# Optimization experiments

Hardware: AMD Instinct MI355X
Metric: run time of the kernel (lower is better)

Reference implementation:

```python
import jax, jax.numpy as jnp
import numpy as np

N, P, VEC, M = 100000, 96, 4, 70000
GROUPS = [27, 8, 8]
K = sum(GROUPS)  # 43
# Replicates the original's use of the LOCAL per-group offset index i_k when
# selecting attention weights in the output accumulation loop.
ATTN_IDX = np.concatenate([np.arange(g) for g in GROUPS]).astype(np.int32)


def setup_inputs() -> dict:
    key = jax.random.key(0)
    ks = jax.random.split(key, 12)
    rng = np.random.default_rng(0)
    # Kernel maps: per offset, M (in_idx, out_idx) pairs; out indices unique per
    # offset (each output point has at most one neighbor at a given offset).
    kmaps = np.stack([
        np.stack([rng.integers(0, N, M), rng.permutation(N)[:M]], axis=1)
        for _ in range(K)
    ]).astype(np.int32)  # [K, M, 2]
    w = lambda k, shape: jax.random.normal(k, shape, jnp.float32) * 0.05
    return dict(
        x=w(ks[0], (N, P)),
        coords=jax.random.uniform(ks[1], (N, 3), jnp.float32, 0.0, 100.0),
        Wq1=w(ks[2], (27, P, P)), gq1=jnp.ones(P), bq1=jnp.zeros(P),
        Wq2=w(ks[3], (27, P, VEC)), gq2=jnp.ones(VEC), bq2=jnp.zeros(VEC),
        Wv=w(ks[4], (27, P, P)), gv=jnp.ones(P), bv=jnp.zeros(P),
        Wp1=w(ks[5], (3, P)), gp1=jnp.ones(P), bp1=jnp.zeros(P),
        Wp2=w(ks[6], (P, VEC)), gp2=jnp.ones(VEC), bp2=jnp.zeros(VEC),
        W1=w(ks[7], (VEC, P)), b1=jnp.zeros(P),
        W2=w(ks[8], (P, VEC)), b2=jnp.zeros(VEC),
        g_out=jnp.ones(P), b_out=jnp.zeros(P),
        kmaps=jnp.asarray(kmaps),
    )


def _bn(x, g, b, eps=1e-5):
    m = x.mean(0)
    v = x.var(0)
    return g * (x - m) * jax.lax.rsqrt(v + eps) + b


def _sparse_conv3(x, W, km27, n):
    # Minkowski kernel-size-3 sparse conv: out[dst] += x[src] @ W[k] per offset.
    def step(acc, kw):
        km, Wk = kw
        return acc.at[km[:, 1]].add(x[km[:, 0]] @ Wk), None
    out, _ = jax.lax.scan(step, jnp.zeros((n, W.shape[-1]), x.dtype), (km27, W))
    return out


def _cbr(x, W, g, b, km27, n):
    return jax.nn.relu(_bn(_sparse_conv3(x, W, km27, n), g, b))


def _forward(x, coords, Wq1, gq1, bq1, Wq2, gq2, bq2, Wv, gv, bv,
             Wp1, gp1, bp1, Wp2, gp2, bp2, W1, b1, W2, b2, g_out, b_out, kmaps):
    n, p = x.shape
    rep = p // VEC  # expand_vec_dim factor
    km27 = kmaps[:27]
    # q branch: two conv3-BN-ReLU stages -> [N, VEC]
    qf = _cbr(_cbr(x, Wq1, gq1, bq1, km27, n), Wq2, gq2, bq2, km27, n)
    # v branch: conv3-BN-ReLU -> [N, P]
    vf = _cbr(x, Wv, gv, bv, km27, n)
    # positional encoding: two 1x1 conv-BN-ReLU on coords -> [N, VEC] -> [N, P]
    pe = jax.nn.relu(_bn(jax.nn.relu(_bn(coords @ Wp1, gp1, bp1)) @ Wp2, gp2, bp2))
    v_f = vf + jnp.repeat(pe, rep, axis=1)

    def attn_step(carry, km):
        src, dst = km[:, 0], km[:, 1]
        # presence mask of offset-k neighbors (scatter of x features, zero elsewhere)
        sm = jnp.zeros((n, p), x.dtype).at[dst].set(x[src])
        mask = jax.lax.stop_gradient((jnp.abs(sm).sum(-1) > 0).astype(x.dtype))  # [N]
        gq = jnp.zeros((n, VEC), x.dtype).at[dst].set(qf[src])
        d = gq - qf * mask[:, None]
        logits = (jax.nn.relu(d @ W1 + b1) @ W2 + b2) * mask[:, None]
        return carry, (logits, mask)

    _, (logits, masks) = jax.lax.scan(attn_step, None, kmaps)  # [K,N,VEC], [K,N]
    attn = jax.nn.softmax(logits, axis=0)  # softmax across the K stacked offsets
    attn_sel = attn[jnp.asarray(ATTN_IDX)]  # replicate local-index selection bug

    def out_step(acc, inp):
        km, mask, a = inp
        nv = jnp.zeros((n, p), x.dtype).at[km[:, 1]].set(v_f[km[:, 0]]) * mask[:, None]
        return acc + nv * jnp.repeat(a, rep, axis=1), None

    out, _ = jax.lax.scan(out_step, jnp.zeros((n, p), x.dtype),
                          (kmaps, masks, attn_sel))
    # out BN + ReLU, residual (inplanes == planes so res = x)
    return jax.nn.relu(_bn(out, g_out, b_out)) + x


def reference(x, coords, Wq1, gq1, bq1, Wq2, gq2, bq2, Wv, gv, bv,
              Wp1, gp1, bp1, Wp2, gp2, bp2, W1, b1, W2, b2, g_out, b_out, kmaps):
    return _forward(x, coords, Wq1, gq1, bq1, Wq2, gq2, bq2, Wv, gv, bv,
                    Wp1, gp1, bp1, Wp2, gp2, bp2, W1, b1, W2, b2,
                    g_out, b_out, kmaps)
```

## Files before the change

kernel.cpp:

```cpp
#include <hip/hip_runtime.h>
#include <math.h>

#define N_  100000
#define P_  96
#define V_  4
#define M_  70000
#define K_  43
#define KC_ 27

typedef unsigned short u16;
typedef __attribute__((ext_vector_type(8))) short bf16x8;
typedef __attribute__((ext_vector_type(4))) float f32x4;
typedef __attribute__((ext_vector_type(16))) float f32x16;

__device__ __forceinline__ u16 f2bf(float f) {
    unsigned int u = __float_as_uint(f);
    u += 0x7fffu + ((u >> 16) & 1u);
    return (u16)(u >> 16);
}
__device__ __forceinline__ float bf2f(u16 h) {
    return __uint_as_float(((unsigned int)h) << 16);
}

__device__ __forceinline__ void gl_lds16(const u16* g, u16* l) {
    __builtin_amdgcn_global_load_lds(
        (const __attribute__((address_space(1))) void*)g,
        (__attribute__((address_space(3))) void*)l, 16, 0, 0);
}

__global__ __launch_bounds__(256) void k_build_srcof(const int* __restrict__ km,
                                                     int* __restrict__ srcOf) {
    int idx = blockIdx.x * 256 + threadIdx.x;
    if (idx >= K_ * M_) return;
    int k = idx / M_;
    int e = idx - k * M_;
    const int* p = km + (size_t)(k * M_ + e) * 2;
    srcOf[(size_t)k * N_ + p[1]] = p[0];
}

__global__ __launch_bounds__(256) void k_rowabs_cvt(const float* __restrict__ x,
                                                    float* __restrict__ rowAbs,
                                                    u16* __restrict__ xb) {
    int row = blockIdx.x * 4 + (threadIdx.x >> 6);
    int lane = threadIdx.x & 63;
    if (row >= N_) return;
    const float* xr = x + (size_t)row * 96;
    float s = 0.f;
    for (int j = lane; j < 96; j += 64) {
        float v = xr[j];
        s += fabsf(v);
        xb[(size_t)row * 96 + j] = f2bf(v);
    }
#pragma unroll
    for (int o = 32; o > 0; o >>= 1) s += __shfl_down(s, o, 64);
    if (lane == 0) rowAbs[row] = s;
}

__global__ __launch_bounds__(256) void k_wt96p(const float* __restrict__ W,
                                               u16* __restrict__ Wp) {
    int idx = blockIdx.x * 256 + threadIdx.x;
    if (idx >= KC_ * 96 * 96) return;
    int k = idx / 9216, rem = idx - k * 9216, n = rem / 96, j = rem - n * 96;
    Wp[(size_t)k * 10240 + n * 104 + j] = f2bf(W[(size_t)k * 9216 + j * 96 + n]);
}

__global__ __launch_bounds__(256) void k_wtB(const float* __restrict__ W,
                                             u16* __restrict__ Bimg) {
    int idx = blockIdx.x * 256 + threadIdx.x;
    if (idx >= 128 * 104) return;
    int n = idx / 104, j = idx - n * 104;
    u16 v = 0;
    if (j < 96 && n < 108) {
        int ks = n >> 2, c = n & 3;
        v = f2bf(W[(size_t)ks * 384 + j * 4 + c]);
    }
    Bimg[idx] = v;
}

__global__ __launch_bounds__(256) void k_w12b(const float* __restrict__ W1,
                                              const float* __restrict__ W2,
                                              u16* __restrict__ w1b,
                                              u16* __restrict__ w2b) {
    int t = blockIdx.x * 256 + threadIdx.x;
    if (t < 96 * 32) {
        int j = t >> 5, c = t & 31;
        w1b[t] = (c < 4) ? f2bf(W1[c * 96 + j]) : (u16)0;
    }
    if (t < 16 * 96) {
        int n = t / 96, j = t - n * 96;
        w2b[t] = (n < 4) ? f2bf(W2[j * 4 + n]) : (u16)0;
    }
}

__global__ __launch_bounds__(384, 3) void k_conv96_dual(
    const u16* __restrict__ xb, const u16* __restrict__ Wqp,
    const u16* __restrict__ Wvp, const int* __restrict__ srcOf,
    u16* __restrict__ yQ, u16* __restrict__ yV,
    float* __restrict__ statsQ, float* __restrict__ statsV) {
    __shared__ u16 sA[192 * 104];
    __shared__ u16 sBq[10240];
    __shared__ u16 sBv[10240];
    const int r0 = blockIdx.x * 192;
    const int t = threadIdx.x;
    const int wv = t / 64, lane = t & 63;
    const int n32 = lane & 31, half = lane >> 5;
    const int ea = t >> 1, jca = (t & 1) * 6;
    f32x16 accq[3], accv[3];
#pragma unroll
    for (int i = 0; i < 3; i++) {
#pragma unroll
        for (int j = 0; j < 16; j++) { accq[i][j] = 0.f; accv[i][j] = 0.f; }
    }

    for (int k = 0; k < KC_; k++) {
        __syncthreads();
        {
            const u16* gq = Wqp + (size_t)k * 10240;
            const u16* gv = Wvp + (size_t)k * 10240;
            for (int i = wv; i < 40; i += 6) {
                int mv = (i >= 20);
                int off = (mv ? i - 20 : i) * 512 + lane * 8;
                gl_lds16((mv ? gv : gq) + off, (mv ? (u16*)sBv : (u16*)sBq) + off);
            }
        }
        {
            int r = r0 + ea;
            int src = (r < N_) ? srcOf[(size_t)k * N_ + r] : -1;
            if (src >= 0) {
                const uint4* sp = (const uint4*)(xb + (size_t)src * 96);
#pragma unroll
                for (int i = 0; i < 6; i++)
                    *(uint4*)(sA + ea * 104 + (jca + i) * 8) = sp[jca + i];
            } else {
                uint4 z = make_uint4(0, 0, 0, 0);
#pragma unroll
                for (int i = 0; i < 6; i++)
                    *(uint4*)(sA + ea * 104 + (jca + i) * 8) = z;
            }
        }
        __syncthreads();
#pragma unroll
        for (int ks = 0; ks < 6; ks++) {
            bf16x8 af = *(const bf16x8*)(sA + (wv * 32 + n32) * 104 + ks * 16 + half * 8);
#pragma unroll
            for (int nt = 0; nt < 3; nt++) {
                bf16x8 bq = *(const bf16x8*)(sBq + (nt * 32 + n32) * 104 + ks * 16 + half * 8);
                accq[nt] = __builtin_amdgcn_mfma_f32_32x32x16_bf16(af, bq, accq[nt], 0, 0, 0);
                bf16x8 bv = *(const bf16x8*)(sBv + (nt * 32 + n32) * 104 + ks * 16 + half * 8);
                accv[nt] = __builtin_amdgcn_mfma_f32_32x32x16_bf16(af, bv, accv[nt], 0, 0, 0);
            }
        }
    }
#pragma unroll
    for (int nt = 0; nt < 3; nt++) {
#pragma unroll
        for (int reg = 0; reg < 16; reg++) {
            int row = (reg & 3) + 8 * (reg >> 2) + 4 * half;
            int r = r0 + wv * 32 + row;
            if (r < N_) {
                yQ[(size_t)r * 96 + nt * 32 + n32] = f2bf(accq[nt][reg]);
                yV[(size_t)r * 96 + nt * 32 + n32] = f2bf(accv[nt][reg]);
            }
        }
    }
    __syncthreads();
    float* sred = (float*)sA;
    for (int pass = 0; pass < 2; pass++) {
        f32x16* acc = pass ? accv : accq;
        float* st = pass ? statsV : statsQ;
#pragma unroll
        for (int nt = 0; nt < 3; nt++) {
            float sv = 0.f, qv = 0.f;
#pragma unroll
            for (int reg = 0; reg < 16; reg++) {
                float a = acc[nt][reg];
                sv += a; qv += a * a;
            }
            sv += __shfl_xor(sv, 32, 64);
            qv += __shfl_xor(qv, 32, 64);
            if (half == 0) {
                sred[wv * 192 + nt * 32 + n32] = sv;
                sred[wv * 192 + 96 + nt * 32 + n32] = qv;
            }
        }
        __syncthreads();
        if (t < 192) {
            float tot = 0.f;
#pragma unroll
            for (int w = 0; w < 6; w++) tot += sred[w * 192 + t];
            atomicAdd(&st[t], tot);
        }
        __syncthreads();
    }
}

__global__ __launch_bounds__(256) void k_proj(
    const u16* __restrict__ xq, const float* __restrict__ stats,
    const float* __restrict__ gg, const float* __restrict__ bb,
    const u16* __restrict__ Bimg, u16* __restrict__ gout) {
    __shared__ u16 sA[128 * 104];
    __shared__ u16 sB[128 * 104];
    __shared__ float sSc[96], sSh[96];
    const int r0 = blockIdx.x * 128;
    const int t = threadIdx.x;
    const int wv = t >> 6, lane = t & 63;
    const int n32 = lane & 31, half = lane >> 5;
    if (t < 96) {
        float mean = stats[t] * (1.f / N_);
        float var = stats[96 + t] * (1.f / N_) - mean * mean;
        float sc = gg[t] * rsqrtf(fmaxf(var, 0.f) + 1e-5f);
        sSc[t] = sc; sSh[t] = bb[t] - mean * sc;
    }
    for (int i = t; i < 1664; i += 256)
        ((uint4*)sB)[i] = ((const uint4*)Bimg)[i];
    __syncthreads();
    {
        int ea = t >> 1, jca = (t & 1) * 6;
        int r = r0 + ea;
        bool ok = (r < N_);
        const u16* xr = xq + (size_t)(ok ? r : 0) * 96;
#pragma unroll
        for (int i = 0; i < 6; i++) {
            int cb = (jca + i) * 8;
            uint4 v = ok ? *(const uint4*)(xr + cb) : make_uint4(0, 0, 0, 0);
            const u16* pv = (const u16*)&v;
            u16 o[8];
#pragma unroll
            for (int e = 0; e < 8; e++) {
                float h = bf2f(pv[e]);
                h = fmaxf(h * sSc[cb + e] + sSh[cb + e], 0.f);
                o[e] = f2bf(h);
            }
            *(uint4*)(sA + ea * 104 + cb) = *(uint4*)o;
        }
    }
    __syncthreads();
    f32x16 acc[4];
#pragma unroll
    for (int i = 0; i < 4; i++)
#pragma unroll
        for (int j = 0; j < 16; j++) acc[i][j] = 0.f;
#pragma unroll
    for (int ks = 0; ks < 6; ks++) {
        bf16x8 af = *(const bf16x8*)(sA + (wv * 32 + n32) * 104 + ks * 16 + half * 8);
#pragma unroll
        for (int nt = 0; nt < 4; nt++) {
            bf16x8 bf = *(const bf16x8*)(sB + (nt * 32 + n32) * 104 + ks * 16 + half * 8);
            acc[nt] = __builtin_amdgcn_mfma_f32_32x32x16_bf16(af, bf, acc[nt], 0, 0, 0);
        }
    }
#pragma unroll
    for (int nt = 0; nt < 4; nt++) {
        int col = nt * 32 + n32;
        if (col < 108) {
#pragma unroll
            for (int reg = 0; reg < 16; reg++) {
                int row = (reg & 3) + 8 * (reg >> 2) + 4 * half;
                int r = r0 + wv * 32 + row;
                if (r < N_) gout[(size_t)r * 108 + col] = f2bf(acc[nt][reg]);
            }
        }
    }
}

__global__ __launch_bounds__(256) void k_gather4(
    const u16* __restrict__ g, const int* __restrict__ srcOf,
    float* __restrict__ qf) {
    int idx = blockIdx.x * 256 + threadIdx.x;
    if (idx >= N_ * 4) return;
    int r = idx >> 2, c = idx & 3;
    float a = 0.f;
    int sv[9]; u16 gv[9];
#pragma unroll 1
    for (int kb = 0; kb < 27; kb += 9) {
#pragma unroll
        for (int j = 0; j < 9; j++)
            sv[j] = srcOf[(size_t)(kb + j) * N_ + r];
#pragma unroll
        for (int j = 0; j < 9; j++) {
            int sc = (sv[j] >= 0) ? sv[j] : 0;
            gv[j] = g[(size_t)sc * 108 + (kb + j) * 4 + c];
        }
#pragma unroll
        for (int j = 0; j < 9; j++)
            if (sv[j] >= 0) a += bf2f(gv[j]);
    }
    qf[idx] = a;
}

__global__ __launch_bounds__(192) void k_bnstats96(const float* __restrict__ xin,
                                                   float* __restrict__ stats) {
    __shared__ float sS[192], sQ[192];
    int t = threadIdx.x;
    int ch = t % 96, half = t / 96;
    float s = 0.f, q = 0.f;
    for (int r = blockIdx.x * 2 + half; r < N_; r += gridDim.x * 2) {
        float v = xin[(size_t)r * 96 + ch];
        s += v; q += v * v;
    }
    sS[t] = s; sQ[t] = q;
    __syncthreads();
    if (t < 96) {
        atomicAdd(&stats[ch], sS[t] + sS[t + 96]);
        atomicAdd(&stats[96 + ch], sQ[t] + sQ[t + 96]);
    }
}

__global__ __launch_bounds__(256) void k_bnstats4(const float* __restrict__ xin,
                                                  float* __restrict__ stats) {
    __shared__ float sS[256], sQ[256];
    int t = threadIdx.x;
    int c = t & 3, sub = t >> 2;
    float s = 0.f, q = 0.f;
    for (int r = blockIdx.x * 64 + sub; r < N_; r += gridDim.x * 64) {
        float v = xin[(size_t)r * 4 + c];
        s += v; q += v * v;
    }
    sS[t] = s; sQ[t] = q;
    __syncthreads();
    for (int off = 128; off >= 4; off >>= 1) {
        if (t < off) { sS[t] += sS[t + off]; sQ[t] += sQ[t + off]; }
        __syncthreads();
    }
    if (t < 4) {
        atomicAdd(&stats[t], sS[t]);
        atomicAdd(&stats[96 + t], sQ[t]);
    }
}

template <int C, int MODE>
__global__ __launch_bounds__(256) void k_bnapply(float* __restrict__ y,
                                                 const float* __restrict__ stats,
                                                 const float* __restrict__ g,
                                                 const float* __restrict__ b,
                                                 const float* __restrict__ aux) {
    int idx = blockIdx.x * 256 + threadIdx.x;
    if (idx >= N_ * C) return;
    int ch = idx % C;
    float mean = stats[ch] * (1.f / N_);
    float var = stats[96 + ch] * (1.f / N_) - mean * mean;
    float scale = g[ch] * rsqrtf(fmaxf(var, 0.f) + 1e-5f);
    float v = (y[idx] - mean) * scale + b[ch];
    v = fmaxf(v, 0.f);
    if (MODE == 2) v += aux[idx];
    y[idx] = v;
}

__global__ __launch_bounds__(256) void k_bnapply96_pe(
    const u16* __restrict__ yin, const float* __restrict__ stats,
    const float* __restrict__ g, const float* __restrict__ b,
    const float* __restrict__ aux, u16* __restrict__ yout) {
    int idx = blockIdx.x * 256 + threadIdx.x;
    if (idx >= N_ * 96) return;
    int ch = idx % 96;
    float mean = stats[ch] * (1.f / N_);
    float var = stats[96 + ch] * (1.f / N_) - mean * mean;
    float scale = g[ch] * rsqrtf(fmaxf(var, 0.f) + 1e-5f);
    float v = (bf2f(yin[idx]) - mean) * scale + b[ch];
    v = fmaxf(v, 0.f);
    int r = idx / 96;
    v += aux[(size_t)r * 4 + (ch / 24)];
    yout[idx] = f2bf(v);
}

__global__ __launch_bounds__(192) void k_pe1s(const float* __restrict__ coords,
                                              const float* __restrict__ Wp1,
                                              u16* __restrict__ out,
                                              float* __restrict__ stats) {
    __shared__ float sS[192], sQ[192];
    int t = threadIdx.x;
    int ch = t % 96, half = t / 96;
    float w0 = Wp1[ch], w1 = Wp1[96 + ch], w2 = Wp1[192 + ch];
    float s = 0.f, q = 0.f;
    for (int r = blockIdx.x * 2 + half; r < N_; r += gridDim.x * 2) {
        float c0 = coords[r * 3], c1 = coords[r * 3 + 1], c2 = coords[r * 3 + 2];
        float v = c0 * w0 + c1 * w1 + c2 * w2;
        out[(size_t)r * 96 + ch] = f2bf(v);
        s += v; q += v * v;
    }
    sS[t] = s; sQ[t] = q;
    __syncthreads();
    if (t < 96) {
        atomicAdd(&stats[ch], sS[t] + sS[t + 96]);
        atomicAdd(&stats[96 + ch], sQ[t] + sQ[t + 96]);
    }
}

__global__ __launch_bounds__(256) void k_pe2b(const u16* __restrict__ hin,
                                              const float* __restrict__ stats,
                                              const float* __restrict__ gp,
                                              const float* __restrict__ bp,
                                              const float* __restrict__ Wp2,
                                              float* __restrict__ out) {
    __shared__ float sSc[96], sSh[96], sW[384];
    int t = threadIdx.x;
    if (t < 96) {
        float mean = stats[t] * (1.f / N_);
        float var = stats[96 + t] * (1.f / N_) - mean * mean;
        float sc = gp[t] * rsqrtf(fmaxf(var, 0.f) + 1e-5f);
        sSc[t] = sc; sSh[t] = bp[t] - mean * sc;
    }
    for (int i = t; i < 384; i += 256) sW[i] = Wp2[i];
    __syncthreads();
    int idx = blockIdx.x * 256 + t;
    if (idx >= N_ * 4) return;
    int r = idx >> 2, c = idx & 3;
    const u16* hr = hin + (size_t)r * 96;
    float acc = 0.f;
#pragma unroll 4
    for (int j = 0; j < 96; j++) {
        float h = fmaxf(bf2f(hr[j]) * sSc[j] + sSh[j], 0.f);
        acc += h * sW[j * 4 + c];
    }
    out[idx] = acc;
}

__global__ __launch_bounds__(256) void k_attn_logits_mfma(
    const float* __restrict__ qf, const int* __restrict__ srcOf,
    const float* __restrict__ rowAbs,
    const u16* __restrict__ w1b, const float* __restrict__ b1,
    const u16* __restrict__ w2b, const float* __restrict__ b2,
    u16* __restrict__ wb) {
    __shared__ u16 hbuf[4][16 * 104];
    __shared__ u16 slogb[32][176];
    __shared__ u16 smk16[32][44];
    const int t = threadIdx.x;
    const int wv = t >> 6, lane = t & 63;
    const int col = lane & 15, quad = lane >> 4;
    const int r0 = blockIdx.x * 32;

    bf16x8 w1f[6];
    float b1v[6];
#pragma unroll
    for (int nt = 0; nt < 6; nt++) {
        w1f[nt] = *(const bf16x8*)(w1b + (nt * 16 + col) * 32 + quad * 8);
        b1v[nt] = b1[nt * 16 + col];
    }
    bf16x8 w2f[3];
#pragma unroll
    for (int kk = 0; kk < 3; kk++)
        w2f[kk] = *(const bf16x8*)(w2b + col * 96 + kk * 32 + quad * 8);
    float b2v = b2[col & 3];

    u16* hb = hbuf[wv];
    for (int tt = 0; tt < 22; tt++) {
        int tileBase = (wv * 22 + tt) * 16;
        bf16x8 af = (bf16x8){0, 0, 0, 0, 0, 0, 0, 0};
        if (quad == 0) {
            int P = tileBase + col;
            int rL = P / 44, k = P - rL * 44;
            int kc = (k < 43) ? k : 42;
            int r = r0 + rL;
            int s = srcOf[(size_t)kc * N_ + r];
            if (k == 43) s = -1;
            int sc = (s >= 0) ? s : 0;
            float mk = (s >= 0 && rowAbs[sc] > 0.f) ? 1.f : 0.f;
            float4 qs = *(const float4*)(qf + (size_t)sc * 4);
            float4 qr = *(const float4*)(qf + (size_t)r * 4);
            af[0] = (short)f2bf((qs.x - qr.x) * mk);
            af[1] = (short)f2bf((qs.y - qr.y) * mk);
            af[2] = (short)f2bf((qs.z - qr.z) * mk);
            af[3] = (short)f2bf((qs.w - qr.w) * mk);
            if (k < 43) smk16[rL][k] = (u16)(mk > 0.f ? 1 : 0);
        }
        f32x4 c1[6];
#pragma unroll
        for (int nt = 0; nt < 6; nt++) {
            c1[nt] = (f32x4){0.f, 0.f, 0.f, 0.f};
            c1[nt] = __builtin_amdgcn_mfma_f32_16x16x32_bf16(af, w1f[nt], c1[nt], 0, 0, 0);
        }
#pragma unroll
        for (int nt = 0; nt < 6; nt++) {
#pragma unroll
            for (int rg = 0; rg < 4; rg++) {
                float h = fmaxf(c1[nt][rg] + b1v[nt], 0.f);
                hb[(quad * 4 + rg) * 104 + nt * 16 + col] = f2bf(h);
            }
        }
        f32x4 acc2 = (f32x4){0.f, 0.f, 0.f, 0.f};
#pragma unroll
        for (int kk = 0; kk < 3; kk++) {
            bf16x8 a2 = *(const bf16x8*)(hb + col * 104 + kk * 32 + quad * 8);
            acc2 = __builtin_amdgcn_mfma_f32_16x16x32_bf16(a2, w2f[kk], acc2, 0, 0, 0);
        }
        if (col < 4) {
#pragma unroll
            for (int rg = 0; rg < 4; rg++) {
                int P = tileBase + quad * 4 + rg;
                int rL = P / 44, k = P - rL * 44;
                if (k < 43) {
                    float mval = (float)smk16[rL][k];
                    slogb[rL][k * 4 + col] = f2bf((acc2[rg] + b2v) * mval);
                }
            }
        }
    }
    __syncthreads();

    if (t < 128) {
        int rL = t >> 2, c = t & 3;
        float mx = 0.f;
        for (int k = 0; k < K_; k++) mx = fmaxf(mx, bf2f(slogb[rL][k * 4 + c]));
        float den = 0.f;
        for (int k = 0; k < K_; k++) den += __expf(bf2f(slogb[rL][k * 4 + c]) - mx);
        float inv = 1.f / den;
        for (int k = 0; k < K_; k++)
            slogb[rL][k * 4 + c] = f2bf(__expf(bf2f(slogb[rL][k * 4 + c]) - mx) * inv);
    }
    __syncthreads();

    for (int p = t; p < 32 * 43; p += 256) {
        int rL = p / 43, k = p - rL * 43;
        int idxk = (k < 27) ? k : ((k < 35) ? (k - 27) : (k - 35));
        u16 mk = smk16[rL][k];
        ushort4 wout = make_ushort4(0, 0, 0, 0);
        if (mk) {
            wout.x = slogb[rL][idxk * 4 + 0];
            wout.y = slogb[rL][idxk * 4 + 1];
            wout.z = slogb[rL][idxk * 4 + 2];
            wout.w = slogb[rL][idxk * 4 + 3];
        }
        *(ushort4*)(wb + ((size_t)(r0 + rL) * 44 + k) * 4) = wout;
    }
}

__global__ __launch_bounds__(256) void k_attn_gather(
    const u16* __restrict__ vfb, const u16* __restrict__ wb,
    const int* __restrict__ srcOf, float* __restrict__ out) {
    int idx = blockIdx.x * 256 + threadIdx.x;
    int r = idx / 24, c4 = idx - r * 24;
    if (r >= N_) return;
    int cg = c4 / 6;
    const u16* wrow = wb + (size_t)r * 176 + cg;
    float a0 = 0.f, a1 = 0.f, a2 = 0.f, a3 = 0.f;
    int sv[8]; float wv[8]; ushort4 vv[8];
#pragma unroll 1
    for (int kb = 0; kb < 40; kb += 8) {
#pragma unroll
        for (int j = 0; j < 8; j++)
            sv[j] = srcOf[(size_t)(kb + j) * N_ + r];
#pragma unroll
        for (int j = 0; j < 8; j++)
            wv[j] = bf2f(wrow[(size_t)(kb + j) * 4]);
#pragma unroll
        for (int j = 0; j < 8; j++) {
            int sc = (sv[j] >= 0) ? sv[j] : 0;
            vv[j] = *(const ushort4*)(vfb + (size_t)sc * 96 + c4 * 4);
        }
#pragma unroll
        for (int j = 0; j < 8; j++) {
            float w = (sv[j] >= 0) ? wv[j] : 0.f;
            a0 += w * bf2f(vv[j].x);
            a1 += w * bf2f(vv[j].y);
            a2 += w * bf2f(vv[j].z);
            a3 += w * bf2f(vv[j].w);
        }
    }
#pragma unroll
    for (int j = 0; j < 3; j++)
        sv[j] = srcOf[(size_t)(40 + j) * N_ + r];
#pragma unroll
    for (int j = 0; j < 3; j++)
        wv[j] = bf2f(wrow[(size_t)(40 + j) * 4]);
#pragma unroll
    for (int j = 0; j < 3; j++) {
        int sc = (sv[j] >= 0) ? sv[j] : 0;
        vv[j] = *(const ushort4*)(vfb + (size_t)sc * 96 + c4 * 4);
    }
#pragma unroll
    for (int j = 0; j < 3; j++) {
        float w = (sv[j] >= 0) ? wv[j] : 0.f;
        a0 += w * bf2f(vv[j].x);
        a1 += w * bf2f(vv[j].y);
        a2 += w * bf2f(vv[j].z);
        a3 += w * bf2f(vv[j].w);
    }
    *(float4*)(out + (size_t)r * 96 + c4 * 4) = make_float4(a0, a1, a2, a3);
}

extern "C" void kernel_launch(void* const* d_in, const int* in_sizes, int n_in,
                              void* d_out, int out_size, void* d_ws, size_t ws_size,
                              hipStream_t stream) {
    const float* x      = (const float*)d_in[0];
    const float* coords = (const float*)d_in[1];
    const float* Wq1 = (const float*)d_in[2];
    const float* gq1 = (const float*)d_in[3];
    const float* bq1 = (const float*)d_in[4];
    const float* Wq2 = (const float*)d_in[5];
    const float* gq2 = (const float*)d_in[6];
    const float* bq2 = (const float*)d_in[7];
    const float* Wv  = (const float*)d_in[8];
    const float* gv  = (const float*)d_in[9];
    const float* bv  = (const float*)d_in[10];
    const float* Wp1 = (const float*)d_in[11];
    const float* gp1 = (const float*)d_in[12];
    const float* bp1 = (const float*)d_in[13];
    const float* Wp2 = (const float*)d_in[14];
    const float* gp2 = (const float*)d_in[15];
    const float* bp2 = (const float*)d_in[16];
    const float* W1  = (const float*)d_in[17];
    const float* b1  = (const float*)d_in[18];
    const float* W2  = (const float*)d_in[19];
    const float* b2  = (const float*)d_in[20];
    const float* g_out = (const float*)d_in[21];
    const float* b_out = (const float*)d_in[22];
    const int* kmaps = (const int*)d_in[23];
    float* out = (float*)d_out;

    char* ws = (char*)d_ws;
    int*   srcOf  = (int*)ws;
    float* rowAbs = (float*)(ws + 17200000);
    u16*   xb     = (u16*)(ws + 17600000);
    u16*   pescr  = (u16*)(ws + 17600000);
    u16*   wbuf   = (u16*)(ws + 17600000);
    u16*   bufQb  = (u16*)(ws + 36800000);
    float* peb    = (float*)(ws + 36800000);
    u16*   Wq1p   = (u16*)(ws + 56000000);
    u16*   Wvp    = (u16*)(ws + 56552960);
    u16*   gbuf   = (u16*)(ws + 56000000);
    u16*   vfb    = (u16*)(ws + 56000000);
    u16*   bufVb  = (u16*)(ws + 77600000);
    u16*   Bimg   = (u16*)(ws + 96800000);
    float* qf     = (float*)(ws + 96800000);
    u16*   w1b    = (u16*)(ws + 98400000);
    u16*   w2b    = (u16*)(ws + 98406144);
    float* stats  = (float*)(ws + 98409216);

    hipMemsetAsync(srcOf, 0xFF, (size_t)K_ * N_ * 4, stream);
    hipMemsetAsync(stats, 0, 6 * 192 * 4, stream);

    k_build_srcof<<<(K_ * M_ + 255) / 256, 256, 0, stream>>>(kmaps, srcOf);
    k_rowabs_cvt<<<N_ / 4, 256, 0, stream>>>(x, rowAbs, xb);
    k_wt96p<<<(KC_ * 9216 + 255) / 256, 256, 0, stream>>>(Wq1, Wq1p);
    k_wt96p<<<(KC_ * 9216 + 255) / 256, 256, 0, stream>>>(Wv, Wvp);
    k_wtB<<<52, 256, 0, stream>>>(Wq2, Bimg);
    k_w12b<<<12, 256, 0, stream>>>(W1, W2, w1b, w2b);

    const int cbD  = (N_ + 191) / 192;
    const int eb96 = N_ * 96 / 256;
    const int eb4  = (N_ * 4 + 255) / 256;

    k_conv96_dual<<<cbD, 384, 0, stream>>>(xb, Wq1p, Wvp, srcOf, bufQb, bufVb,
                                           stats + 0 * 192, stats + 4 * 192);

    k_proj<<<(N_ + 127) / 128, 256, 0, stream>>>(bufQb, stats + 0 * 192, gq1, bq1,
                                                 Bimg, gbuf);
    k_gather4<<<eb4, 256, 0, stream>>>(gbuf, srcOf, qf);
    k_bnstats4<<<512, 256, 0, stream>>>(qf, stats + 1 * 192);
    k_bnapply<4, 0><<<eb4, 256, 0, stream>>>(qf, stats + 1 * 192, gq2, bq2, nullptr);

    k_pe1s<<<512, 192, 0, stream>>>(coords, Wp1, pescr, stats + 2 * 192);
    k_pe2b<<<eb4, 256, 0, stream>>>(pescr, stats + 2 * 192, gp1, bp1, Wp2, peb);
    k_bnstats4<<<512, 256, 0, stream>>>(peb, stats + 3 * 192);
    k_bnapply<4, 0><<<eb4, 256, 0, stream>>>(peb, stats + 3 * 192, gp2, bp2, nullptr);

    k_bnapply96_pe<<<eb96, 256, 0, stream>>>(bufVb, stats + 4 * 192, gv, bv, peb, vfb);

    k_attn_logits_mfma<<<N_ / 32, 256, 0, stream>>>(qf, srcOf, rowAbs, w1b, b1, w2b, b2, wbuf);
    k_attn_gather<<<(N_ * 24) / 256, 256, 0, stream>>>(vfb, wbuf, srcOf, out);

    k_bnstats96<<<512, 192, 0, stream>>>(out, stats + 5 * 192);
    k_bnapply<96, 2><<<eb96, 256, 0, stream>>>(out, stats + 5 * 192, g_out, b_out, x);
}
```

Baseline: 889.0 us.

## Fuse attention softmax with value gather and fold small BN applies into consumers

Merges the attention-logit kernel and the gather kernel, so the softmax weights stay in shared memory instead of making a round trip through a global buffer. The 4-channel BN+ReLU applies for the q and positional-encoding branches are removed and recomputed inline in their consumers, which saves two launches and two small passes over memory. In exchange, each attention block now runs three gather passes with a serialized tail after the softmax, which may reduce memory-level parallelism compared with the separate gather grid. The q BN is recomputed for every neighbor lookup, adding some ALU work.

```diff
diff --git a/kernel.cpp b/kernel.cpp
--- a/kernel.cpp
+++ b/kernel.cpp
@@ -349,7 +349,9 @@
 __global__ __launch_bounds__(256) void k_bnapply96_pe(
     const u16* __restrict__ yin, const float* __restrict__ stats,
     const float* __restrict__ g, const float* __restrict__ b,
-    const float* __restrict__ aux, u16* __restrict__ yout) {
+    const float* __restrict__ aux, const float* __restrict__ statsP,
+    const float* __restrict__ gp2, const float* __restrict__ bp2,
+    u16* __restrict__ yout) {
     int idx = blockIdx.x * 256 + threadIdx.x;
     if (idx >= N_ * 96) return;
     int ch = idx % 96;
@@ -359,8 +361,12 @@
     float v = (bf2f(yin[idx]) - mean) * scale + b[ch];
     v = fmaxf(v, 0.f);
     int r = idx / 96;
-    v += aux[(size_t)r * 4 + (ch / 24)];
-    yout[idx] = f2bf(v);
+    int c = ch / 24;
+    float pm = statsP[c] * (1.f / N_);
+    float pv = statsP[96 + c] * (1.f / N_) - pm * pm;
+    float psc = gp2[c] * rsqrtf(fmaxf(pv, 0.f) + 1e-5f);
+    float pe = fmaxf(aux[(size_t)r * 4 + c] * psc + (bp2[c] - pm * psc), 0.f);
+    yout[idx] = f2bf(v + pe);
 }
 
 __global__ __launch_bounds__(192) void k_pe1s(const float* __restrict__ coords,
@@ -415,12 +421,14 @@
     out[idx] = acc;
 }
 
-__global__ __launch_bounds__(256) void k_attn_logits_mfma(
+__global__ __launch_bounds__(256) void k_attn_fused(
     const float* __restrict__ qf, const int* __restrict__ srcOf,
     const float* __restrict__ rowAbs,
     const u16* __restrict__ w1b, const float* __restrict__ b1,
     const u16* __restrict__ w2b, const float* __restrict__ b2,
-    u16* __restrict__ wb) {
+    const float* __restrict__ statsQ, const float* __restrict__ gq2,
+    const float* __restrict__ bq2,
+    const u16* __restrict__ vfb, float* __restrict__ out) {
     __shared__ u16 hbuf[4][16 * 104];
     __shared__ u16 slogb[32][176];
     __shared__ u16 smk16[32][44];
@@ -428,6 +436,15 @@
     const int wv = t >> 6, lane = t & 63;
     const int col = lane & 15, quad = lane >> 4;
     const int r0 = blockIdx.x * 32;
+
+    float qsc[4], qsh[4];
+#pragma unroll
+    for (int c = 0; c < 4; c++) {
+        float mean = statsQ[c] * (1.f / N_);
+        float var = statsQ[96 + c] * (1.f / N_) - mean * mean;
+        float s = gq2[c] * rsqrtf(fmaxf(var, 0.f) + 1e-5f);
+        qsc[c] = s; qsh[c] = bq2[c] - mean * s;
+    }
 
     bf16x8 w1f[6];
     float b1v[6];
@@ -457,6 +474,14 @@
             float mk = (s >= 0 && rowAbs[sc] > 0.f) ? 1.f : 0.f;
             float4 qs = *(const float4*)(qf + (size_t)sc * 4);
             float4 qr = *(const float4*)(qf + (size_t)r * 4);
+            qs.x = fmaxf(qs.x * qsc[0] + qsh[0], 0.f);
+            qs.y = fmaxf(qs.y * qsc[1] + qsh[1], 0.f);
+            qs.z = fmaxf(qs.z * qsc[2] + qsh[2], 0.f);
+            qs.w = fmaxf(qs.w * qsc[3] + qsh[3], 0.f);
+            qr.x = fmaxf(qr.x * qsc[0] + qsh[0], 0.f);
+            qr.y = fmaxf(qr.y * qsc[1] + qsh[1], 0.f);
+            qr.z = fmaxf(qr.z * qsc[2] + qsh[2], 0.f);
+            qr.w = fmaxf(qr.w * qsc[3] + qsh[3], 0.f);
             af[0] = (short)f2bf((qs.x - qr.x) * mk);
             af[1] = (short)f2bf((qs.y - qr.y) * mk);
             af[2] = (short)f2bf((qs.z - qr.z) * mk);
@@ -509,73 +534,62 @@
     }
     __syncthreads();
 
-    for (int p = t; p < 32 * 43; p += 256) {
-        int rL = p / 43, k = p - rL * 43;
-        int idxk = (k < 27) ? k : ((k < 35) ? (k - 27) : (k - 35));
-        u16 mk = smk16[rL][k];
-        ushort4 wout = make_ushort4(0, 0, 0, 0);
-        if (mk) {
-            wout.x = slogb[rL][idxk * 4 + 0];
-            wout.y = slogb[rL][idxk * 4 + 1];
-            wout.z = slogb[rL][idxk * 4 + 2];
-            wout.w = slogb[rL][idxk * 4 + 3];
-        }
-        *(ushort4*)(wb + ((size_t)(r0 + rL) * 44 + k) * 4) = wout;
-    }
-}
-
-__global__ __launch_bounds__(256) void k_attn_gather(
-    const u16* __restrict__ vfb, const u16* __restrict__ wb,
-    const int* __restrict__ srcOf, float* __restrict__ out) {
-    int idx = blockIdx.x * 256 + threadIdx.x;
-    int r = idx / 24, c4 = idx - r * 24;
-    if (r >= N_) return;
-    int cg = c4 / 6;
-    const u16* wrow = wb + (size_t)r * 176 + cg;
-    float a0 = 0.f, a1 = 0.f, a2 = 0.f, a3 = 0.f;
-    int sv[8]; float wv[8]; ushort4 vv[8];
 #pragma unroll 1
-    for (int kb = 0; kb < 40; kb += 8) {
-#pragma unroll
-        for (int j = 0; j < 8; j++)
-            sv[j] = srcOf[(size_t)(kb + j) * N_ + r];
-#pragma unroll
-        for (int j = 0; j < 8; j++)
-            wv[j] = bf2f(wrow[(size_t)(kb + j) * 4]);
-#pragma unroll
-        for (int j = 0; j < 8; j++) {
+    for (int pass = 0; pass < 3; pass++) {
+        int p = pass * 256 + t;
+        int rL = p / 24, c4 = p - rL * 24;
+        int r = r0 + rL;
+        int cg = c4 / 6;
+        float a0 = 0.f, a1 = 0.f, a2 = 0.f, a3 = 0.f;
+        int sv[8]; float wv8[8]; ushort4 vv[8];
+#pragma unroll 1
+        for (int kb = 0; kb < 40; kb += 8) {
+#pragma unroll
+            for (int j = 0; j < 8; j++)
+                sv[j] = srcOf[(size_t)(kb + j) * N_ + r];
+#pragma unroll
+            for (int j = 0; j < 8; j++) {
+                int k = kb + j;
+                int idxk = (k < 27) ? k : ((k < 35) ? (k - 27) : (k - 35));
+                wv8[j] = smk16[rL][k] ? bf2f(slogb[rL][idxk * 4 + cg]) : 0.f;
+            }
+#pragma unroll
+            for (int j = 0; j < 8; j++) {
+                int sc = (sv[j] >= 0) ? sv[j] : 0;
+                vv[j] = *(const ushort4*)(vfb + (size_t)sc * 96 + c4 * 4);
+            }
+#pragma unroll
+            for (int j = 0; j < 8; j++) {
+                float w = wv8[j];
+                a0 += w * bf2f(vv[j].x);
+                a1 += w * bf2f(vv[j].y);
+                a2 += w * bf2f(vv[j].z);
+                a3 += w * bf2f(vv[j].w);
+            }
+        }
+#pragma unroll
+        for (int j = 0; j < 3; j++)
+            sv[j] = srcOf[(size_t)(40 + j) * N_ + r];
+#pragma unroll
+        for (int j = 0; j < 3; j++) {
+            int k = 40 + j;
+            wv8[j] = smk16[rL][k] ? bf2f(slogb[rL][(k - 35) * 4 + cg]) : 0.f;
+        }
+#pragma unroll
+        for (int j = 0; j < 3; j++) {
             int sc = (sv[j] >= 0) ? sv[j] : 0;
             vv[j] = *(const ushort4*)(vfb + (size_t)sc * 96 + c4 * 4);
         }
 #pragma unroll
-        for (int j = 0; j < 8; j++) {
-            float w = (sv[j] >= 0) ? wv[j] : 0.f;
+        for (int j = 0; j < 3; j++) {
+            float w = wv8[j];
             a0 += w * bf2f(vv[j].x);
             a1 += w * bf2f(vv[j].y);
             a2 += w * bf2f(vv[j].z);
             a3 += w * bf2f(vv[j].w);
         }
-    }
-#pragma unroll
-    for (int j = 0; j < 3; j++)
-        sv[j] = srcOf[(size_t)(40 + j) * N_ + r];
-#pragma unroll
-    for (int j = 0; j < 3; j++)
-        wv[j] = bf2f(wrow[(size_t)(40 + j) * 4]);
-#pragma unroll
-    for (int j = 0; j < 3; j++) {
-        int sc = (sv[j] >= 0) ? sv[j] : 0;
-        vv[j] = *(const ushort4*)(vfb + (size_t)sc * 96 + c4 * 4);
-    }
-#pragma unroll
-    for (int j = 0; j < 3; j++) {
-        float w = (sv[j] >= 0) ? wv[j] : 0.f;
-        a0 += w * bf2f(vv[j].x);
-        a1 += w * bf2f(vv[j].y);
-        a2 += w * bf2f(vv[j].z);
-        a3 += w * bf2f(vv[j].w);
-    }
-    *(float4*)(out + (size_t)r * 96 + c4 * 4) = make_float4(a0, a1, a2, a3);
+        *(float4*)(out + (size_t)r * 96 + c4 * 4) = make_float4(a0, a1, a2, a3);
+    }
 }
 
 extern "C" void kernel_launch(void* const* d_in, const int* in_sizes, int n_in,
@@ -612,7 +626,6 @@
     float* rowAbs = (float*)(ws + 17200000);
     u16*   xb     = (u16*)(ws + 17600000);
     u16*   pescr  = (u16*)(ws + 17600000);
-    u16*   wbuf   = (u16*)(ws + 17600000);
     u16*   bufQb  = (u16*)(ws + 36800000);
     float* peb    = (float*)(ws + 36800000);
     u16*   Wq1p   = (u16*)(ws + 56000000);
@@ -647,17 +660,16 @@
                                                  Bimg, gbuf);
     k_gather4<<<eb4, 256, 0, stream>>>(gbuf, srcOf, qf);
     k_bnstats4<<<512, 256, 0, stream>>>(qf, stats + 1 * 192);
-    k_bnapply<4, 0><<<eb4, 256, 0, stream>>>(qf, stats + 1 * 192, gq2, bq2, nullptr);
 
     k_pe1s<<<512, 192, 0, stream>>>(coords, Wp1, pescr, stats + 2 * 192);
     k_pe2b<<<eb4, 256, 0, stream>>>(pescr, stats + 2 * 192, gp1, bp1, Wp2, peb);
     k_bnstats4<<<512, 256, 0, stream>>>(peb, stats + 3 * 192);
-    k_bnapply<4, 0><<<eb4, 256, 0, stream>>>(peb, stats + 3 * 192, gp2, bp2, nullptr);
-
-    k_bnapply96_pe<<<eb96, 256, 0, stream>>>(bufVb, stats + 4 * 192, gv, bv, peb, vfb);
-
-    k_attn_logits_mfma<<<N_ / 32, 256, 0, stream>>>(qf, srcOf, rowAbs, w1b, b1, w2b, b2, wbuf);
-    k_attn_gather<<<(N_ * 24) / 256, 256, 0, stream>>>(vfb, wbuf, srcOf, out);
+
+    k_bnapply96_pe<<<eb96, 256, 0, stream>>>(bufVb, stats + 4 * 192, gv, bv, peb,
+                                             stats + 3 * 192, gp2, bp2, vfb);
+
+    k_attn_fused<<<N_ / 32, 256, 0, stream>>>(qf, srcOf, rowAbs, w1b, b1, w2b, b2,
+                                              stats + 1 * 192, gq2, bq2, vfb, out);
 
     k_bnstats96<<<512, 192, 0, stream>>>(out, stats + 5 * 192);
     k_bnapply<96, 2><<<eb96, 256, 0, stream>>>(out, stats + 5 * 192, g_out, b_out, x);
```

Result: slower. 919.2 us (+3.4%).

## Quantize gathered activations to int8 with per-row scales and fold BN applies

Applied to the files above, without the earlier changes.

The input x is stored as per-row int8 with a float scale, and the conv gather dequantizes it to bf16 in LDS. The v features are stored as per-row uint8 (post-ReLU) for the attention gather. The q2 and pe2 BN-apply kernels are removed and folded into their consumers. This cuts gather bandwidth in the conv and attention-gather stages and saves two launches, at the cost of lower precision (8-bit) and extra dequantization ALU work.

```diff
diff --git a/kernel.cpp b/kernel.cpp
--- a/kernel.cpp
+++ b/kernel.cpp
@@ -9,6 +9,7 @@
 #define KC_ 27
 
 typedef unsigned short u16;
+typedef unsigned char u8;
 typedef __attribute__((ext_vector_type(8))) short bf16x8;
 typedef __attribute__((ext_vector_type(4))) float f32x4;
 typedef __attribute__((ext_vector_type(16))) float f32x16;
@@ -38,22 +39,29 @@
     srcOf[(size_t)k * N_ + p[1]] = p[0];
 }
 
-__global__ __launch_bounds__(256) void k_rowabs_cvt(const float* __restrict__ x,
-                                                    float* __restrict__ rowAbs,
-                                                    u16* __restrict__ xb) {
+__global__ __launch_bounds__(256) void k_rowabs_cvti8(const float* __restrict__ x,
+                                                      float* __restrict__ rowAbs,
+                                                      u8* __restrict__ xq8) {
     int row = blockIdx.x * 4 + (threadIdx.x >> 6);
     int lane = threadIdx.x & 63;
     if (row >= N_) return;
     const float* xr = x + (size_t)row * 96;
-    float s = 0.f;
-    for (int j = lane; j < 96; j += 64) {
-        float v = xr[j];
-        s += fabsf(v);
-        xb[(size_t)row * 96 + j] = f2bf(v);
-    }
-#pragma unroll
-    for (int o = 32; o > 0; o >>= 1) s += __shfl_down(s, o, 64);
+    float v0 = xr[lane < 96 ? lane : 0];
+    if (lane >= 96) v0 = 0.f;
+    float v1 = (lane + 64 < 96) ? xr[lane + 64] : 0.f;
+    float s = fabsf(v0) + fabsf(v1);
+    float m = fmaxf(fabsf(v0), fabsf(v1));
+#pragma unroll
+    for (int o = 32; o > 0; o >>= 1) {
+        s += __shfl_down(s, o, 64);
+        m = fmaxf(m, __shfl_xor(m, o, 64));
+    }
     if (lane == 0) rowAbs[row] = s;
+    float inv = (m > 0.f) ? 127.f / m : 0.f;
+    u8* orow = xq8 + (size_t)row * 128;
+    orow[lane] = (u8)(signed char)(int)rintf(v0 * inv);
+    if (lane + 64 < 96) orow[lane + 64] = (u8)(signed char)(int)rintf(v1 * inv);
+    if (lane == 0) *(float*)(orow + 96) = (m > 0.f) ? m * (1.f / 127.f) : 0.f;
 }
 
 __global__ __launch_bounds__(256) void k_wt96p(const float* __restrict__ W,
@@ -93,7 +101,7 @@
 }
 
 __global__ __launch_bounds__(384, 3) void k_conv96_dual(
-    const u16* __restrict__ xb, const u16* __restrict__ Wqp,
+    const u8* __restrict__ xq8, const u16* __restrict__ Wqp,
     const u16* __restrict__ Wvp, const int* __restrict__ srcOf,
     u16* __restrict__ yQ, u16* __restrict__ yV,
     float* __restrict__ statsQ, float* __restrict__ statsV) {
@@ -104,7 +112,7 @@
     const int t = threadIdx.x;
     const int wv = t / 64, lane = t & 63;
     const int n32 = lane & 31, half = lane >> 5;
-    const int ea = t >> 1, jca = (t & 1) * 6;
+    const int ea = t >> 1, jb = (t & 1) * 48;
     f32x16 accq[3], accv[3];
 #pragma unroll
     for (int i = 0; i < 3; i++) {
@@ -126,16 +134,31 @@
         {
             int r = r0 + ea;
             int src = (r < N_) ? srcOf[(size_t)k * N_ + r] : -1;
+            u16* dst = sA + ea * 104 + jb;
             if (src >= 0) {
-                const uint4* sp = (const uint4*)(xb + (size_t)src * 96);
-#pragma unroll
-                for (int i = 0; i < 6; i++)
-                    *(uint4*)(sA + ea * 104 + (jca + i) * 8) = sp[jca + i];
+                const u8* rp = xq8 + (size_t)src * 128;
+                float sc = *(const float*)(rp + 96);
+                const uint4* sp = (const uint4*)(rp + jb);
+#pragma unroll
+                for (int i = 0; i < 3; i++) {
+                    uint4 v = sp[i];
+                    unsigned int w4[4] = {v.x, v.y, v.z, v.w};
+                    u16 o[16];
+#pragma unroll
+                    for (int q = 0; q < 4; q++)
+#pragma unroll
+                        for (int b = 0; b < 4; b++) {
+                            int iv = (int)(signed char)((w4[q] >> (8 * b)) & 0xffu);
+                            o[q * 4 + b] = f2bf((float)iv * sc);
+                        }
+                    *(uint4*)(dst + i * 16) = *(uint4*)(o);
+                    *(uint4*)(dst + i * 16 + 8) = *(uint4*)(o + 8);
+                }
             } else {
                 uint4 z = make_uint4(0, 0, 0, 0);
 #pragma unroll
                 for (int i = 0; i < 6; i++)
-                    *(uint4*)(sA + ea * 104 + (jca + i) * 8) = z;
+                    *(uint4*)(dst + i * 8) = z;
             }
         }
         __syncthreads();
@@ -346,21 +369,50 @@
     y[idx] = v;
 }
 
-__global__ __launch_bounds__(256) void k_bnapply96_pe(
+__global__ __launch_bounds__(192) void k_bnv8(
     const u16* __restrict__ yin, const float* __restrict__ stats,
     const float* __restrict__ g, const float* __restrict__ b,
-    const float* __restrict__ aux, u16* __restrict__ yout) {
-    int idx = blockIdx.x * 256 + threadIdx.x;
-    if (idx >= N_ * 96) return;
-    int ch = idx % 96;
+    const float* __restrict__ aux, const float* __restrict__ statsP,
+    const float* __restrict__ gp2, const float* __restrict__ bp2,
+    u8* __restrict__ vq8) {
+    __shared__ float red[2][96];
+    __shared__ float ssc[2];
+    int t = threadIdx.x;
+    int half = t / 96, ch = t - half * 96;
+    int r = blockIdx.x * 2 + half;
     float mean = stats[ch] * (1.f / N_);
     float var = stats[96 + ch] * (1.f / N_) - mean * mean;
-    float scale = g[ch] * rsqrtf(fmaxf(var, 0.f) + 1e-5f);
-    float v = (bf2f(yin[idx]) - mean) * scale + b[ch];
+    float sc = g[ch] * rsqrtf(fmaxf(var, 0.f) + 1e-5f);
+    float v = (bf2f(yin[(size_t)r * 96 + ch]) - mean) * sc + b[ch];
     v = fmaxf(v, 0.f);
-    int r = idx / 96;
-    v += aux[(size_t)r * 4 + (ch / 24)];
-    yout[idx] = f2bf(v);
+    int c = ch / 24;
+    float pm = statsP[c] * (1.f / N_);
+    float pv = statsP[96 + c] * (1.f / N_) - pm * pm;
+    float psc = gp2[c] * rsqrtf(fmaxf(pv, 0.f) + 1e-5f);
+    v += fmaxf(aux[(size_t)r * 4 + c] * psc + (bp2[c] - pm * psc), 0.f);
+    red[half][ch] = v;
+    __syncthreads();
+    if (ch < 48) red[half][ch] = fmaxf(red[half][ch], red[half][ch + 48]);
+    __syncthreads();
+    if (ch < 24) red[half][ch] = fmaxf(red[half][ch], red[half][ch + 24]);
+    __syncthreads();
+    if (ch < 12) red[half][ch] = fmaxf(red[half][ch], red[half][ch + 12]);
+    __syncthreads();
+    if (ch < 6)  red[half][ch] = fmaxf(red[half][ch], red[half][ch + 6]);
+    __syncthreads();
+    if (ch == 0) {
+        float m = red[half][0];
+#pragma unroll
+        for (int i = 1; i < 6; i++) m = fmaxf(m, red[half][i]);
+        ssc[half] = m;
+    }
+    __syncthreads();
+    float m = ssc[half];
+    float inv = (m > 0.f) ? 255.f / m : 0.f;
+    float q = rintf(v * inv);
+    vq8[(size_t)r * 128 + ch] = (u8)fminf(q, 255.f);
+    if (ch == 0) *(float*)(vq8 + (size_t)r * 128 + 96) =
+        (m > 0.f) ? m * (1.f / 255.f) : 0.f;
 }
 
 __global__ __launch_bounds__(192) void k_pe1s(const float* __restrict__ coords,
@@ -420,6 +472,8 @@
     const float* __restrict__ rowAbs,
     const u16* __restrict__ w1b, const float* __restrict__ b1,
     const u16* __restrict__ w2b, const float* __restrict__ b2,
+    const float* __restrict__ statsQ, const float* __restrict__ gq2,
+    const float* __restrict__ bq2,
     u16* __restrict__ wb) {
     __shared__ u16 hbuf[4][16 * 104];
     __shared__ u16 slogb[32][176];
@@ -428,6 +482,15 @@
     const int wv = t >> 6, lane = t & 63;
     const int col = lane & 15, quad = lane >> 4;
     const int r0 = blockIdx.x * 32;
+
+    float qsc[4], qsh[4];
+#pragma unroll
+    for (int c = 0; c < 4; c++) {
+        float mean = statsQ[c] * (1.f / N_);
+        float var = statsQ[96 + c] * (1.f / N_) - mean * mean;
+        float s = gq2[c] * rsqrtf(fmaxf(var, 0.f) + 1e-5f);
+        qsc[c] = s; qsh[c] = bq2[c] - mean * s;
+    }
 
     bf16x8 w1f[6];
     float b1v[6];
@@ -457,6 +520,14 @@
             float mk = (s >= 0 && rowAbs[sc] > 0.f) ? 1.f : 0.f;
             float4 qs = *(const float4*)(qf + (size_t)sc * 4);
             float4 qr = *(const float4*)(qf + (size_t)r * 4);
+            qs.x = fmaxf(qs.x * qsc[0] + qsh[0], 0.f);
+            qs.y = fmaxf(qs.y * qsc[1] + qsh[1], 0.f);
+            qs.z = fmaxf(qs.z * qsc[2] + qsh[2], 0.f);
+            qs.w = fmaxf(qs.w * qsc[3] + qsh[3], 0.f);
+            qr.x = fmaxf(qr.x * qsc[0] + qsh[0], 0.f);
+            qr.y = fmaxf(qr.y * qsc[1] + qsh[1], 0.f);
+            qr.z = fmaxf(qr.z * qsc[2] + qsh[2], 0.f);
+            qr.w = fmaxf(qr.w * qsc[3] + qsh[3], 0.f);
             af[0] = (short)f2bf((qs.x - qr.x) * mk);
             af[1] = (short)f2bf((qs.y - qr.y) * mk);
             af[2] = (short)f2bf((qs.z - qr.z) * mk);
@@ -525,7 +596,7 @@
 }
 
 __global__ __launch_bounds__(256) void k_attn_gather(
-    const u16* __restrict__ vfb, const u16* __restrict__ wb,
+    const u8* __restrict__ vq8, const u16* __restrict__ wb,
     const int* __restrict__ srcOf, float* __restrict__ out) {
     int idx = blockIdx.x * 256 + threadIdx.x;
     int r = idx / 24, c4 = idx - r * 24;
@@ -533,7 +604,7 @@
     int cg = c4 / 6;
     const u16* wrow = wb + (size_t)r * 176 + cg;
     float a0 = 0.f, a1 = 0.f, a2 = 0.f, a3 = 0.f;
-    int sv[8]; float wv[8]; ushort4 vv[8];
+    int sv[8]; float wv[8]; unsigned int vv[8]; float scv[8];
 #pragma unroll 1
     for (int kb = 0; kb < 40; kb += 8) {
 #pragma unroll
@@ -545,15 +616,17 @@
 #pragma unroll
         for (int j = 0; j < 8; j++) {
             int sc = (sv[j] >= 0) ? sv[j] : 0;
-            vv[j] = *(const ushort4*)(vfb + (size_t)sc * 96 + c4 * 4);
+            const u8* rp = vq8 + (size_t)sc * 128;
+            vv[j] = *(const unsigned int*)(rp + c4 * 4);
+            scv[j] = *(const float*)(rp + 96);
         }
 #pragma unroll
         for (int j = 0; j < 8; j++) {
-            float w = (sv[j] >= 0) ? wv[j] : 0.f;
-            a0 += w * bf2f(vv[j].x);
-            a1 += w * bf2f(vv[j].y);
-            a2 += w * bf2f(vv[j].z);
-            a3 += w * bf2f(vv[j].w);
+            float w = (sv[j] >= 0) ? wv[j] * scv[j] : 0.f;
+            a0 += w * (float)(vv[j] & 0xffu);
+            a1 += w * (float)((vv[j] >> 8) & 0xffu);
+            a2 += w * (float)((vv[j] >> 16) & 0xffu);
+            a3 += w * (float)((vv[j] >> 24) & 0xffu);
         }
     }
 #pragma unroll
@@ -565,15 +638,17 @@
 #pragma unroll
     for (int j = 0; j < 3; j++) {
         int sc = (sv[j] >= 0) ? sv[j] : 0;
-        vv[j] = *(const ushort4*)(vfb + (size_t)sc * 96 + c4 * 4);
+        const u8* rp = vq8 + (size_t)sc * 128;
+        vv[j] = *(const unsigned int*)(rp + c4 * 4);
+        scv[j] = *(const float*)(rp + 96);
     }
 #pragma unroll
     for (int j = 0; j < 3; j++) {
-        float w = (sv[j] >= 0) ? wv[j] : 0.f;
-        a0 += w * bf2f(vv[j].x);
-        a1 += w * bf2f(vv[j].y);
-        a2 += w * bf2f(vv[j].z);
-        a3 += w * bf2f(vv[j].w);
+        float w = (sv[j] >= 0) ? wv[j] * scv[j] : 0.f;
+        a0 += w * (float)(vv[j] & 0xffu);
+        a1 += w * (float)((vv[j] >> 8) & 0xffu);
+        a2 += w * (float)((vv[j] >> 16) & 0xffu);
+        a3 += w * (float)((vv[j] >> 24) & 0xffu);
     }
     *(float4*)(out + (size_t)r * 96 + c4 * 4) = make_float4(a0, a1, a2, a3);
 }
@@ -610,27 +685,27 @@
     char* ws = (char*)d_ws;
     int*   srcOf  = (int*)ws;
     float* rowAbs = (float*)(ws + 17200000);
-    u16*   xb     = (u16*)(ws + 17600000);
-    u16*   pescr  = (u16*)(ws + 17600000);
-    u16*   wbuf   = (u16*)(ws + 17600000);
-    u16*   bufQb  = (u16*)(ws + 36800000);
-    float* peb    = (float*)(ws + 36800000);
-    u16*   Wq1p   = (u16*)(ws + 56000000);
-    u16*   Wvp    = (u16*)(ws + 56552960);
-    u16*   gbuf   = (u16*)(ws + 56000000);
-    u16*   vfb    = (u16*)(ws + 56000000);
-    u16*   bufVb  = (u16*)(ws + 77600000);
-    u16*   Bimg   = (u16*)(ws + 96800000);
-    float* qf     = (float*)(ws + 96800000);
-    u16*   w1b    = (u16*)(ws + 98400000);
-    u16*   w2b    = (u16*)(ws + 98406144);
-    float* stats  = (float*)(ws + 98409216);
+    float* stats  = (float*)(ws + 17600000);
+    u16*   w1b    = (u16*)(ws + 17604608);
+    u16*   w2b    = (u16*)(ws + 17610752);
+    u16*   Bimg   = (u16*)(ws + 17613824);
+    u16*   Wq1p   = (u16*)(ws + 17640448);
+    u16*   Wvp    = (u16*)(ws + 18193408);
+    u8*    xq8    = (u8*)(ws + 18746368);
+    u16*   bufQb  = (u16*)(ws + 31546368);
+    u16*   bufVb  = (u16*)(ws + 50746368);
+    u16*   gbuf   = (u16*)(ws + 69946368);
+    float* qf     = (float*)(ws + 91546368);
+    float* peb    = (float*)(ws + 93146368);
+    u16*   pescr  = (u16*)(ws + 18746368);
+    u8*    vq8    = (u8*)(ws + 69946368);
+    u16*   wbuf   = (u16*)(ws + 18746368);
 
     hipMemsetAsync(srcOf, 0xFF, (size_t)K_ * N_ * 4, stream);
     hipMemsetAsync(stats, 0, 6 * 192 * 4, stream);
 
     k_build_srcof<<<(K_ * M_ + 255) / 256, 256, 0, stream>>>(kmaps, srcOf);
-    k_rowabs_cvt<<<N_ / 4, 256, 0, stream>>>(x, rowAbs, xb);
+    k_rowabs_cvti8<<<N_ / 4, 256, 0, stream>>>(x, rowAbs, xq8);
     k_wt96p<<<(KC_ * 9216 + 255) / 256, 256, 0, stream>>>(Wq1, Wq1p);
     k_wt96p<<<(KC_ * 9216 + 255) / 256, 256, 0, stream>>>(Wv, Wvp);
     k_wtB<<<52, 256, 0, stream>>>(Wq2, Bimg);
@@ -638,26 +713,28 @@
 
     const int cbD  = (N_ + 191) / 192;
     const int eb96 = N_ * 96 / 256;
+    const int eb24 = (N_ * 24) / 256;
     const int eb4  = (N_ * 4 + 255) / 256;
 
-    k_conv96_dual<<<cbD, 384, 0, stream>>>(xb, Wq1p, Wvp, srcOf, bufQb, bufVb,
+    k_conv96_dual<<<cbD, 384, 0, stream>>>(xq8, Wq1p, Wvp, srcOf, bufQb, bufVb,
                                            stats + 0 * 192, stats + 4 * 192);
 
     k_proj<<<(N_ + 127) / 128, 256, 0, stream>>>(bufQb, stats + 0 * 192, gq1, bq1,
                                                  Bimg, gbuf);
     k_gather4<<<eb4, 256, 0, stream>>>(gbuf, srcOf, qf);
     k_bnstats4<<<512, 256, 0, stream>>>(qf, stats + 1 * 192);
-    k_bnapply<4, 0><<<eb4, 256, 0, stream>>>(qf, stats + 1 * 192, gq2, bq2, nullptr);
 
     k_pe1s<<<512, 192, 0, stream>>>(coords, Wp1, pescr, stats + 2 * 192);
     k_pe2b<<<eb4, 256, 0, stream>>>(pescr, stats + 2 * 192, gp1, bp1, Wp2, peb);
     k_bnstats4<<<512, 256, 0, stream>>>(peb, stats + 3 * 192);
-    k_bnapply<4, 0><<<eb4, 256, 0, stream>>>(peb, stats + 3 * 192, gp2, bp2, nullptr);
-
-    k_bnapply96_pe<<<eb96, 256, 0, stream>>>(bufVb, stats + 4 * 192, gv, bv, peb, vfb);
-
-    k_attn_logits_mfma<<<N_ / 32, 256, 0, stream>>>(qf, srcOf, rowAbs, w1b, b1, w2b, b2, wbuf);
-    k_attn_gather<<<(N_ * 24) / 256, 256, 0, stream>>>(vfb, wbuf, srcOf, out);
+
+    k_bnv8<<<N_ / 2, 192, 0, stream>>>(bufVb, stats + 4 * 192, gv, bv, peb,
+                                       stats + 3 * 192, gp2, bp2, vq8);
+
+    k_attn_logits_mfma<<<N_ / 32, 256, 0, stream>>>(qf, srcOf, rowAbs, w1b, b1,
+                                                    w2b, b2, stats + 1 * 192,
+                                                    gq2, bq2, wbuf);
+    k_attn_gather<<<eb24, 256, 0, stream>>>(vq8, wbuf, srcOf, out);
 
     k_bnstats96<<<512, 192, 0, stream>>>(out, stats + 5 * 192);
     k_bnapply<96, 2><<<eb96, 256, 0, stream>>>(out, stats + 5 * 192, g_out, b_out, x);
```

Result: slower. 912.4 us (+2.6%).
